# Optimization experiments

Hardware: AMD Instinct MI355X
Metric: run time of the kernel (lower is better)

Reference implementation:

```python
import jax, jax.numpy as jnp
import numpy as np

N_SUPPORT = 131072
NUM_CLASSES = 1024
D = 512
NUM_LEVELS = 3
LN_EPS = 1e-5


def setup_inputs() -> dict:
    key = jax.random.key(0)
    ks = jax.random.split(key, 10)
    s = 1.0 / np.sqrt(D)
    return {
        "support_features": jax.random.normal(ks[0], (N_SUPPORT, D), dtype=jnp.float32),
        "support_labels": jax.random.randint(ks[1], (N_SUPPORT,), 0, NUM_CLASSES, dtype=jnp.int32),
        "W1": jax.random.normal(ks[2], (NUM_LEVELS, D, D), dtype=jnp.float32) * s,
        "b1": jnp.zeros((NUM_LEVELS, D), dtype=jnp.float32),
        "ln_gamma": jnp.ones((NUM_LEVELS, D), dtype=jnp.float32),
        "ln_beta": jnp.zeros((NUM_LEVELS, D), dtype=jnp.float32),
        "W2": jax.random.normal(ks[3], (NUM_LEVELS, D, D), dtype=jnp.float32) * s,
        "b2": jnp.zeros((NUM_LEVELS, D), dtype=jnp.float32),
        "level_temperatures": jnp.ones((NUM_LEVELS,), dtype=jnp.float32),
    }


def _prototype_level(x, labels, w1, bb1, gamma, beta, w2, bb2, counts):
    # MLP: Linear -> LayerNorm -> ReLU -> (Dropout=identity, eval) -> Linear
    h = x @ w1 + bb1                                   # [N, D]
    mu = jnp.mean(h, axis=-1, keepdims=True)
    var = jnp.mean(jnp.square(h - mu), axis=-1, keepdims=True)
    h = (h - mu) * jax.lax.rsqrt(var + LN_EPS) * gamma + beta
    h = jax.nn.relu(h)
    h = h @ w2 + bb2                                   # [N, D]
    # per-class mean prototype (segment mean)
    sums = jax.ops.segment_sum(h, labels, num_segments=NUM_CLASSES)  # [C, D]
    return sums / counts


def reference(support_features, support_labels, W1, b1, ln_gamma, ln_beta, W2, b2, level_temperatures):
    labels = support_labels.astype(jnp.int32)
    counts = jax.ops.segment_sum(
        jnp.ones((support_features.shape[0],), dtype=support_features.dtype),
        labels, num_segments=NUM_CLASSES)
    counts = jnp.maximum(counts, 1.0)[:, None]         # [C, 1]

    level_protos = jax.vmap(
        lambda w1, bb1, g, bt, w2, bb2: _prototype_level(
            support_features, labels, w1, bb1, g, bt, w2, bb2, counts)
    )(W1, b1, ln_gamma, ln_beta, W2, b2)               # [L, C, D]

    level_weights = jax.nn.softmax(level_temperatures)  # [L]
    final_prototypes = jnp.einsum('l,lcd->cd', level_weights, level_protos)
    return final_prototypes
```

## Files before the change

kernel.cpp:

```cpp
#include <hip/hip_runtime.h>
#include <hip/hip_bf16.h>
#include <cstdint>

#define N_SUPPORT 131072
#define NUM_CLASSES 1024
#define DIM 512
#define LN_EPS 1e-5f

typedef __attribute__((ext_vector_type(8))) short bf16x8;
typedef __attribute__((ext_vector_type(4))) float f32x4;

__device__ __forceinline__ unsigned short f2bf(float f) {
  union { float f; uint32_t u; } c; c.f = f;
  uint32_t u = c.u;
  u += 0x7fffu + ((u >> 16) & 1u);
  return (unsigned short)(u >> 16);
}

__device__ __forceinline__ void gload16(const void* g, void* l) {
  __builtin_amdgcn_global_load_lds((const __attribute__((address_space(1))) void*)g,
                                   (__attribute__((address_space(3))) void*)l,
                                   16, 0, 0);
}

__global__ void k_hist(const int* __restrict__ labels, int* __restrict__ counts) {
  const int i = blockIdx.x * 256 + threadIdx.x;
  atomicAdd(&counts[labels[i]], 1);
}

__global__ void k_scan(const int* __restrict__ counts, int* __restrict__ offs,
                       float* __restrict__ invc) {
  __shared__ int tmp[1024];
  const int t = threadIdx.x;
  const int myc = counts[t];
  tmp[t] = myc;
  __syncthreads();
  for (int o = 1; o < 1024; o <<= 1) {
    int v = (t >= o) ? tmp[t - o] : 0;
    __syncthreads();
    tmp[t] += v;
    __syncthreads();
  }
  offs[t] = tmp[t] - myc;
  invc[t] = 1.0f / (float)max(myc, 1);
}

__global__ void k_scatter(const int* __restrict__ labels, const int* __restrict__ offs,
                          int* __restrict__ cursor, int* __restrict__ sorted) {
  const int i = blockIdx.x * 256 + threadIdx.x;
  const int c = labels[i];
  const int p = atomicAdd(&cursor[c], 1);
  sorted[offs[c] + p] = i;
}

__global__ void k_cast_sorted(const float* __restrict__ x, const int* __restrict__ sorted,
                              const int* __restrict__ labels,
                              unsigned short* __restrict__ xb, int* __restrict__ scls) {
  const int p = blockIdx.x * 4 + (threadIdx.x >> 6);
  const int src = sorted[p];
  const int k = (threadIdx.x & 63) * 8;
  const float* xr = x + (size_t)src * DIM + k;
  float4 a = *(const float4*)(xr);
  float4 b = *(const float4*)(xr + 4);
  uint4 o;
  o.x = (uint32_t)f2bf(a.x) | ((uint32_t)f2bf(a.y) << 16);
  o.y = (uint32_t)f2bf(a.z) | ((uint32_t)f2bf(a.w) << 16);
  o.z = (uint32_t)f2bf(b.x) | ((uint32_t)f2bf(b.y) << 16);
  o.w = (uint32_t)f2bf(b.z) | ((uint32_t)f2bf(b.w) << 16);
  *(uint4*)(xb + (size_t)p * DIM + k) = o;
  if ((threadIdx.x & 63) == 0) scls[p] = labels[src];
}

__global__ void k_prep_w1t(const float* __restrict__ w1, unsigned short* __restrict__ w1t) {
  const int idx = blockIdx.x * 256 + threadIdx.x;
  const int l = idx >> 18;
  const int rem = idx & 262143;
  const int k = rem >> 9;
  const int n = rem & 511;
  w1t[((size_t)l * 512 + n) * 512 + k] = f2bf(w1[idx]);
}

__global__ __launch_bounds__(256, 2) void k_gemm1lnred(
    const unsigned short* __restrict__ Xb, const unsigned short* __restrict__ W1T,
    const float* __restrict__ b1, const float* __restrict__ gamma, const float* __restrict__ beta,
    const int* __restrict__ scls_g, float* __restrict__ M, int l)
{
  __shared__ unsigned short sX[64 * 32];
  __shared__ unsigned short sW[512 * 32];
  __shared__ float wsum[4][64];
  __shared__ float wsq[4][64];
  __shared__ float smean[64];
  __shared__ float srstd[64];
  __shared__ int scls[64];
  __shared__ int run_start[65];
  __shared__ int run_cls[64];
  __shared__ int nruns_s;

  const int t = threadIdx.x;
  const int wv = t >> 6;
  const int lane = t & 63;
  const int lr = lane & 15;
  const int lq = lane >> 4;
  const int row0 = blockIdx.x * 64;

  const unsigned short* Wl = W1T + (size_t)l * 512 * 512;

  f32x4 acc[4][8];
  #pragma unroll
  for (int i = 0; i < 4; ++i)
    #pragma unroll
    for (int j = 0; j < 8; ++j) acc[i][j] = (f32x4){0.f, 0.f, 0.f, 0.f};

  const int xrow = t >> 2;
  const int ko8 = (t & 3) * 8;
  const unsigned short* xg = Xb + (size_t)(row0 + xrow) * 512 + ko8;
  unsigned short* sXw = sX + wv * 512;

  if (t < 64) scls[t] = scls_g[row0 + t];

  for (int ks = 0; ks < 16; ++ks) {
    const int kk = ks * 32;
    gload16(xg + kk, sXw);
    #pragma unroll
    for (int i = 0; i < 8; ++i) {
      const int n = i * 64 + (t >> 2);
      gload16(Wl + (size_t)n * 512 + kk + ko8, sW + (i * 256 + wv * 64) * 8);
    }
    __syncthreads();

    bf16x8 a[4], b[8];
    #pragma unroll
    for (int rf = 0; rf < 4; ++rf)
      a[rf] = *(const bf16x8*)(sX + (rf * 16 + lr) * 32 + lq * 8);
    #pragma unroll
    for (int cf = 0; cf < 8; ++cf)
      b[cf] = *(const bf16x8*)(sW + (wv * 128 + cf * 16 + lr) * 32 + lq * 8);

    #pragma unroll
    for (int rf = 0; rf < 4; ++rf)
      #pragma unroll
      for (int cf = 0; cf < 8; ++cf)
        acc[rf][cf] = __builtin_amdgcn_mfma_f32_16x16x32_bf16(a[rf], b[cf], acc[rf][cf], 0, 0, 0);
    __syncthreads();
  }

  float b1v[8], gv[8], bv[8];
  #pragma unroll
  for (int cf = 0; cf < 8; ++cf) {
    const int col = wv * 128 + cf * 16 + lr;
    b1v[cf] = b1[l * 512 + col];
    gv[cf] = gamma[l * 512 + col];
    bv[cf] = beta[l * 512 + col];
  }
  #pragma unroll
  for (int rf = 0; rf < 4; ++rf)
    #pragma unroll
    for (int cf = 0; cf < 8; ++cf)
      #pragma unroll
      for (int j = 0; j < 4; ++j) acc[rf][cf][j] += b1v[cf];

  #pragma unroll
  for (int rf = 0; rf < 4; ++rf) {
    #pragma unroll
    for (int j = 0; j < 4; ++j) {
      float s = 0.f, q = 0.f;
      #pragma unroll
      for (int cf = 0; cf < 8; ++cf) { float v = acc[rf][cf][j]; s += v; q += v * v; }
      #pragma unroll
      for (int m = 8; m >= 1; m >>= 1) { s += __shfl_xor(s, m, 16); q += __shfl_xor(q, m, 16); }
      if (lr == 0) { const int row = rf * 16 + lq * 4 + j; wsum[wv][row] = s; wsq[wv][row] = q; }
    }
  }
  __syncthreads();
  if (t < 64) {
    const float s = wsum[0][t] + wsum[1][t] + wsum[2][t] + wsum[3][t];
    const float q = wsq[0][t] + wsq[1][t] + wsq[2][t] + wsq[3][t];
    const float mean = s * (1.0f / 512.0f);
    const float var = q * (1.0f / 512.0f) - mean * mean;
    smean[t] = mean;
    srstd[t] = rsqrtf(var + LN_EPS);
  }
  if (t == 0) {
    int n = 0;
    run_start[0] = 0;
    run_cls[0] = scls[0];
    for (int r = 1; r < 64; ++r) {
      if (scls[r] != scls[r - 1]) { ++n; run_start[n] = r; run_cls[n] = scls[r]; }
    }
    nruns_s = n + 1;
    run_start[n + 1] = 64;
  }
  __syncthreads();

  #pragma unroll
  for (int rf = 0; rf < 4; ++rf) {
    #pragma unroll
    for (int j = 0; j < 4; ++j) {
      const int row = rf * 16 + lq * 4 + j;
      const float mean = smean[row], rs = srstd[row];
      #pragma unroll
      for (int cf = 0; cf < 8; ++cf) {
        float v = (acc[rf][cf][j] - mean) * rs * gv[cf] + bv[cf];
        acc[rf][cf][j] = fmaxf(v, 0.f);
      }
    }
  }

  const int nruns = nruns_s;
  float* Ml = M + (size_t)l * NUM_CLASSES * DIM;
  for (int r = 0; r < nruns; ++r) {
    const int rs = run_start[r], re = run_start[r + 1];
    const int cls = run_cls[r];
    float p[8];
    #pragma unroll
    for (int cf = 0; cf < 8; ++cf) p[cf] = 0.f;
    #pragma unroll
    for (int rf = 0; rf < 4; ++rf) {
      #pragma unroll
      for (int j = 0; j < 4; ++j) {
        const int row = rf * 16 + lq * 4 + j;
        if (row >= rs && row < re) {
          #pragma unroll
          for (int cf = 0; cf < 8; ++cf) p[cf] += acc[rf][cf][j];
        }
      }
    }
    #pragma unroll
    for (int cf = 0; cf < 8; ++cf) {
      p[cf] += __shfl_xor(p[cf], 16);
      p[cf] += __shfl_xor(p[cf], 32);
    }
    if (lq == 0) {
      #pragma unroll
      for (int cf = 0; cf < 8; ++cf)
        atomicAdd(&Ml[(size_t)cls * DIM + wv * 128 + cf * 16 + lr], p[cf]);
    }
  }
}

__global__ void k_final(const float* __restrict__ M, const float* __restrict__ W2,
                        const float* __restrict__ b2, const float* __restrict__ temps,
                        const float* __restrict__ invc, float* __restrict__ out)
{
  __shared__ float sA[64][17];
  __shared__ float sB[16][65];
  const int t = threadIdx.x;
  const int tx = t & 15, ty = t >> 4;
  const int bcol = blockIdx.x * 64;
  const int brow = blockIdx.y * 64;

  const float t0 = temps[0], t1 = temps[1], t2 = temps[2];
  const float mx = fmaxf(t0, fmaxf(t1, t2));
  const float e0 = expf(t0 - mx), e1 = expf(t1 - mx), e2 = expf(t2 - mx);
  const float inv = 1.f / (e0 + e1 + e2);
  const float w[3] = {e0 * inv, e1 * inv, e2 * inv};

  float acc[4][4] = {};
  for (int l = 0; l < 3; ++l) {
    for (int k0 = 0; k0 < 512; k0 += 16) {
      __syncthreads();
      #pragma unroll
      for (int i = 0; i < 4; ++i) {
        const int e = i * 256 + t;
        const int r = e >> 4, k = e & 15;
        sA[r][k] = M[((size_t)l * 1024 + brow + r) * 512 + k0 + k] * (w[l] * invc[brow + r]);
      }
      #pragma unroll
      for (int i = 0; i < 4; ++i) {
        const int e = i * 256 + t;
        const int r = e >> 6, nn = e & 63;
        sB[r][nn] = W2[((size_t)l * 512 + k0 + r) * 512 + bcol + nn];
      }
      __syncthreads();
      #pragma unroll
      for (int kk = 0; kk < 16; ++kk) {
        float a[4], b[4];
        #pragma unroll
        for (int i = 0; i < 4; ++i) a[i] = sA[ty * 4 + i][kk];
        #pragma unroll
        for (int j = 0; j < 4; ++j) b[j] = sB[kk][tx * 4 + j];
        #pragma unroll
        for (int i = 0; i < 4; ++i)
          #pragma unroll
          for (int j = 0; j < 4; ++j) acc[i][j] += a[i] * b[j];
      }
    }
  }
  #pragma unroll
  for (int j = 0; j < 4; ++j) {
    const int col = bcol + tx * 4 + j;
    const float bias = w[0] * b2[col] + w[1] * b2[512 + col] + w[2] * b2[1024 + col];
    #pragma unroll
    for (int i = 0; i < 4; ++i)
      out[(size_t)(brow + ty * 4 + i) * 512 + col] = acc[i][j] + bias;
  }
}

extern "C" void kernel_launch(void* const* d_in, const int* in_sizes, int n_in,
                              void* d_out, int out_size, void* d_ws, size_t ws_size,
                              hipStream_t stream)
{
  const float* X = (const float*)d_in[0];
  const int* labels = (const int*)d_in[1];
  const float* W1 = (const float*)d_in[2];
  const float* b1 = (const float*)d_in[3];
  const float* gamma = (const float*)d_in[4];
  const float* beta = (const float*)d_in[5];
  const float* W2 = (const float*)d_in[6];
  const float* b2 = (const float*)d_in[7];
  const float* temps = (const float*)d_in[8];
  float* out = (float*)d_out;

  char* ws = (char*)d_ws;
  size_t off = 0;
  auto alloc = [&](size_t bytes) -> char* {
    char* p = ws + off;
    off += (bytes + 255) & ~(size_t)255;
    return p;
  };
  unsigned short* Xb = (unsigned short*)alloc((size_t)N_SUPPORT * DIM * 2);
  unsigned short* W1T = (unsigned short*)alloc((size_t)3 * 512 * 512 * 2);
  float* M = (float*)alloc((size_t)3 * 1024 * 512 * 4);
  int* counts = (int*)alloc(2048 * 4);
  int* cursor = counts + 1024;
  int* offs = (int*)alloc(1024 * 4);
  float* invc = (float*)alloc(1024 * 4);
  int* sorted = (int*)alloc((size_t)N_SUPPORT * 4);
  int* scls = (int*)alloc((size_t)N_SUPPORT * 4);

  hipMemsetAsync(counts, 0, 2048 * 4, stream);
  hipMemsetAsync(M, 0, (size_t)3 * 1024 * 512 * 4, stream);
  k_hist<<<512, 256, 0, stream>>>(labels, counts);
  k_scan<<<1, 1024, 0, stream>>>(counts, offs, invc);
  k_scatter<<<512, 256, 0, stream>>>(labels, offs, cursor, sorted);
  k_cast_sorted<<<32768, 256, 0, stream>>>(X, sorted, labels, Xb, scls);
  k_prep_w1t<<<3072, 256, 0, stream>>>(W1, W1T);
  for (int l = 0; l < 3; ++l) {
    k_gemm1lnred<<<2048, 256, 0, stream>>>(Xb, W1T, b1, gamma, beta, scls, M, l);
  }
  k_final<<<dim3(8, 16), 256, 0, stream>>>(M, W2, b2, temps, invc, out);
}
```

Baseline: 954.3 us.

## Pre-tile X and W1 into MFMA-friendly layout, merge level launches, split final GEMM

Writes X and W1 into a k-slice-major tiled bf16 layout, so each global-to-LDS load in the GEMM is fully contiguous and the LDS fragment reads avoid the strided row layout. The three per-level GEMM launches become one 2D grid with the level on x, so the three blocks sharing an X tile run close together and can reuse it from L2. The final GEMM is split across levels in blockIdx.z and accumulates into a zeroed output with atomics, which raises parallelism from 128 blocks to 384. The costs are an extra memset, float atomic nondeterminism, and less coalesced stores in the cast and transpose kernels.

```diff
diff --git a/kernel.cpp b/kernel.cpp
--- a/kernel.cpp
+++ b/kernel.cpp
@@ -55,38 +55,57 @@
 
 __global__ void k_cast_sorted(const float* __restrict__ x, const int* __restrict__ sorted,
                               const int* __restrict__ labels,
-                              unsigned short* __restrict__ xb, int* __restrict__ scls) {
-  const int p = blockIdx.x * 4 + (threadIdx.x >> 6);
+                              unsigned short* __restrict__ xbt, int* __restrict__ scls) {
+  const int tile = blockIdx.x;
+  const int t = threadIdx.x;
+  const int rr = t & 63, ksl = t >> 6;
+  const int p = tile * 64 + rr;
   const int src = sorted[p];
-  const int k = (threadIdx.x & 63) * 8;
-  const float* xr = x + (size_t)src * DIM + k;
-  float4 a = *(const float4*)(xr);
-  float4 b = *(const float4*)(xr + 4);
+  if (t < 64) scls[p] = labels[src];
+  const float* xr = x + (size_t)src * DIM;
+  #pragma unroll
+  for (int kb = 0; kb < 4; ++kb) {
+    const int ks = kb * 4 + ksl;
+    float4 f[8];
+    #pragma unroll
+    for (int i = 0; i < 8; ++i) f[i] = *(const float4*)(xr + ks * 32 + i * 4);
+    #pragma unroll
+    for (int g = 0; g < 4; ++g) {
+      uint4 o;
+      o.x = (uint32_t)f2bf(f[g * 2].x) | ((uint32_t)f2bf(f[g * 2].y) << 16);
+      o.y = (uint32_t)f2bf(f[g * 2].z) | ((uint32_t)f2bf(f[g * 2].w) << 16);
+      o.z = (uint32_t)f2bf(f[g * 2 + 1].x) | ((uint32_t)f2bf(f[g * 2 + 1].y) << 16);
+      o.w = (uint32_t)f2bf(f[g * 2 + 1].z) | ((uint32_t)f2bf(f[g * 2 + 1].w) << 16);
+      *(uint4*)(xbt + ((size_t)(tile * 64 + ks * 4 + g)) * 512 + rr * 8) = o;
+    }
+  }
+}
+
+__global__ void k_prep_w1t(const float* __restrict__ w1, unsigned short* __restrict__ w1t) {
+  const int i = blockIdx.x * 256 + threadIdx.x;
+  const int l = i >> 15;
+  const int ks = (i >> 11) & 15;
+  const int g = (i >> 9) & 3;
+  const int n = i & 511;
+  const float* src = w1 + ((size_t)l * 512 + ks * 32 + g * 8) * 512 + n;
+  unsigned short v[8];
+  #pragma unroll
+  for (int e = 0; e < 8; ++e) v[e] = f2bf(src[(size_t)e * 512]);
   uint4 o;
-  o.x = (uint32_t)f2bf(a.x) | ((uint32_t)f2bf(a.y) << 16);
-  o.y = (uint32_t)f2bf(a.z) | ((uint32_t)f2bf(a.w) << 16);
-  o.z = (uint32_t)f2bf(b.x) | ((uint32_t)f2bf(b.y) << 16);
-  o.w = (uint32_t)f2bf(b.z) | ((uint32_t)f2bf(b.w) << 16);
-  *(uint4*)(xb + (size_t)p * DIM + k) = o;
-  if ((threadIdx.x & 63) == 0) scls[p] = labels[src];
-}
-
-__global__ void k_prep_w1t(const float* __restrict__ w1, unsigned short* __restrict__ w1t) {
-  const int idx = blockIdx.x * 256 + threadIdx.x;
-  const int l = idx >> 18;
-  const int rem = idx & 262143;
-  const int k = rem >> 9;
-  const int n = rem & 511;
-  w1t[((size_t)l * 512 + n) * 512 + k] = f2bf(w1[idx]);
+  o.x = (uint32_t)v[0] | ((uint32_t)v[1] << 16);
+  o.y = (uint32_t)v[2] | ((uint32_t)v[3] << 16);
+  o.z = (uint32_t)v[4] | ((uint32_t)v[5] << 16);
+  o.w = (uint32_t)v[6] | ((uint32_t)v[7] << 16);
+  *(uint4*)(w1t + (size_t)i * 8) = o;
 }
 
 __global__ __launch_bounds__(256, 2) void k_gemm1lnred(
-    const unsigned short* __restrict__ Xb, const unsigned short* __restrict__ W1T,
+    const unsigned short* __restrict__ XbT, const unsigned short* __restrict__ W1T,
     const float* __restrict__ b1, const float* __restrict__ gamma, const float* __restrict__ beta,
-    const int* __restrict__ scls_g, float* __restrict__ M, int l)
+    const int* __restrict__ scls_g, float* __restrict__ M)
 {
-  __shared__ unsigned short sX[64 * 32];
-  __shared__ unsigned short sW[512 * 32];
+  __shared__ unsigned short sX[4 * 64 * 8];
+  __shared__ unsigned short sW[4 * 512 * 8];
   __shared__ float wsum[4][64];
   __shared__ float wsq[4][64];
   __shared__ float smean[64];
@@ -101,9 +120,12 @@
   const int lane = t & 63;
   const int lr = lane & 15;
   const int lq = lane >> 4;
-  const int row0 = blockIdx.x * 64;
-
-  const unsigned short* Wl = W1T + (size_t)l * 512 * 512;
+  const int l = blockIdx.x;
+  const int tile = blockIdx.y;
+  const int row0 = tile * 64;
+
+  const unsigned short* xsrc = XbT + (size_t)tile * 32768;
+  const unsigned short* wsrc = W1T + (size_t)l * 262144;
 
   f32x4 acc[4][8];
   #pragma unroll
@@ -111,30 +133,23 @@
     #pragma unroll
     for (int j = 0; j < 8; ++j) acc[i][j] = (f32x4){0.f, 0.f, 0.f, 0.f};
 
-  const int xrow = t >> 2;
-  const int ko8 = (t & 3) * 8;
-  const unsigned short* xg = Xb + (size_t)(row0 + xrow) * 512 + ko8;
+  if (t < 64) scls[t] = scls_g[row0 + t];
+
   unsigned short* sXw = sX + wv * 512;
-
-  if (t < 64) scls[t] = scls_g[row0 + t];
-
   for (int ks = 0; ks < 16; ++ks) {
-    const int kk = ks * 32;
-    gload16(xg + kk, sXw);
-    #pragma unroll
-    for (int i = 0; i < 8; ++i) {
-      const int n = i * 64 + (t >> 2);
-      gload16(Wl + (size_t)n * 512 + kk + ko8, sW + (i * 256 + wv * 64) * 8);
-    }
+    gload16(xsrc + (size_t)ks * 2048 + t * 8, sXw);
+    #pragma unroll
+    for (int i = 0; i < 8; ++i)
+      gload16(wsrc + (size_t)ks * 16384 + (i * 256 + t) * 8, sW + (i * 256 + wv * 64) * 8);
     __syncthreads();
 
     bf16x8 a[4], b[8];
     #pragma unroll
     for (int rf = 0; rf < 4; ++rf)
-      a[rf] = *(const bf16x8*)(sX + (rf * 16 + lr) * 32 + lq * 8);
+      a[rf] = *(const bf16x8*)(sX + (lq * 64 + rf * 16 + lr) * 8);
     #pragma unroll
     for (int cf = 0; cf < 8; ++cf)
-      b[cf] = *(const bf16x8*)(sW + (wv * 128 + cf * 16 + lr) * 32 + lq * 8);
+      b[cf] = *(const bf16x8*)(sW + (lq * 512 + wv * 128 + cf * 16 + lr) * 8);
 
     #pragma unroll
     for (int rf = 0; rf < 4; ++rf)
@@ -248,51 +263,52 @@
   const int tx = t & 15, ty = t >> 4;
   const int bcol = blockIdx.x * 64;
   const int brow = blockIdx.y * 64;
+  const int l = blockIdx.z;
 
   const float t0 = temps[0], t1 = temps[1], t2 = temps[2];
   const float mx = fmaxf(t0, fmaxf(t1, t2));
   const float e0 = expf(t0 - mx), e1 = expf(t1 - mx), e2 = expf(t2 - mx);
   const float inv = 1.f / (e0 + e1 + e2);
   const float w[3] = {e0 * inv, e1 * inv, e2 * inv};
+  const float wl = w[l];
 
   float acc[4][4] = {};
-  for (int l = 0; l < 3; ++l) {
-    for (int k0 = 0; k0 < 512; k0 += 16) {
-      __syncthreads();
-      #pragma unroll
-      for (int i = 0; i < 4; ++i) {
-        const int e = i * 256 + t;
-        const int r = e >> 4, k = e & 15;
-        sA[r][k] = M[((size_t)l * 1024 + brow + r) * 512 + k0 + k] * (w[l] * invc[brow + r]);
-      }
-      #pragma unroll
-      for (int i = 0; i < 4; ++i) {
-        const int e = i * 256 + t;
-        const int r = e >> 6, nn = e & 63;
-        sB[r][nn] = W2[((size_t)l * 512 + k0 + r) * 512 + bcol + nn];
-      }
-      __syncthreads();
-      #pragma unroll
-      for (int kk = 0; kk < 16; ++kk) {
-        float a[4], b[4];
+  for (int k0 = 0; k0 < 512; k0 += 16) {
+    __syncthreads();
+    #pragma unroll
+    for (int i = 0; i < 4; ++i) {
+      const int e = i * 256 + t;
+      const int r = e >> 4, k = e & 15;
+      sA[r][k] = M[((size_t)l * 1024 + brow + r) * 512 + k0 + k] * (wl * invc[brow + r]);
+    }
+    #pragma unroll
+    for (int i = 0; i < 4; ++i) {
+      const int e = i * 256 + t;
+      const int r = e >> 6, nn = e & 63;
+      sB[r][nn] = W2[((size_t)l * 512 + k0 + r) * 512 + bcol + nn];
+    }
+    __syncthreads();
+    #pragma unroll
+    for (int kk = 0; kk < 16; ++kk) {
+      float a[4], b[4];
+      #pragma unroll
+      for (int i = 0; i < 4; ++i) a[i] = sA[ty * 4 + i][kk];
+      #pragma unroll
+      for (int j = 0; j < 4; ++j) b[j] = sB[kk][tx * 4 + j];
+      #pragma unroll
+      for (int i = 0; i < 4; ++i)
         #pragma unroll
-        for (int i = 0; i < 4; ++i) a[i] = sA[ty * 4 + i][kk];
-        #pragma unroll
-        for (int j = 0; j < 4; ++j) b[j] = sB[kk][tx * 4 + j];
-        #pragma unroll
-        for (int i = 0; i < 4; ++i)
-          #pragma unroll
-          for (int j = 0; j < 4; ++j) acc[i][j] += a[i] * b[j];
-      }
+        for (int j = 0; j < 4; ++j) acc[i][j] += a[i] * b[j];
     }
   }
   #pragma unroll
   for (int j = 0; j < 4; ++j) {
     const int col = bcol + tx * 4 + j;
-    const float bias = w[0] * b2[col] + w[1] * b2[512 + col] + w[2] * b2[1024 + col];
+    const float bias = (l == 0)
+        ? (w[0] * b2[col] + w[1] * b2[512 + col] + w[2] * b2[1024 + col]) : 0.f;
     #pragma unroll
     for (int i = 0; i < 4; ++i)
-      out[(size_t)(brow + ty * 4 + i) * 512 + col] = acc[i][j] + bias;
+      atomicAdd(&out[(size_t)(brow + ty * 4 + i) * 512 + col], acc[i][j] + bias);
   }
 }
 
@@ -318,7 +334,7 @@
     off += (bytes + 255) & ~(size_t)255;
     return p;
   };
-  unsigned short* Xb = (unsigned short*)alloc((size_t)N_SUPPORT * DIM * 2);
+  unsigned short* XbT = (unsigned short*)alloc((size_t)N_SUPPORT * DIM * 2);
   unsigned short* W1T = (unsigned short*)alloc((size_t)3 * 512 * 512 * 2);
   float* M = (float*)alloc((size_t)3 * 1024 * 512 * 4);
   int* counts = (int*)alloc(2048 * 4);
@@ -330,13 +346,12 @@
 
   hipMemsetAsync(counts, 0, 2048 * 4, stream);
   hipMemsetAsync(M, 0, (size_t)3 * 1024 * 512 * 4, stream);
+  hipMemsetAsync(out, 0, (size_t)NUM_CLASSES * DIM * 4, stream);
   k_hist<<<512, 256, 0, stream>>>(labels, counts);
   k_scan<<<1, 1024, 0, stream>>>(counts, offs, invc);
   k_scatter<<<512, 256, 0, stream>>>(labels, offs, cursor, sorted);
-  k_cast_sorted<<<32768, 256, 0, stream>>>(X, sorted, labels, Xb, scls);
-  k_prep_w1t<<<3072, 256, 0, stream>>>(W1, W1T);
-  for (int l = 0; l < 3; ++l) {
-    k_gemm1lnred<<<2048, 256, 0, stream>>>(Xb, W1T, b1, gamma, beta, scls, M, l);
-  }
-  k_final<<<dim3(8, 16), 256, 0, stream>>>(M, W2, b2, temps, invc, out);
-}
+  k_cast_sorted<<<2048, 256, 0, stream>>>(X, sorted, labels, XbT, scls);
+  k_prep_w1t<<<384, 256, 0, stream>>>(W1, W1T);
+  k_gemm1lnred<<<dim3(3, 2048), 256, 0, stream>>>(XbT, W1T, b1, gamma, beta, scls, M);
+  k_final<<<dim3(8, 16, 3), 256, 0, stream>>>(M, W2, b2, temps, invc, out);
+}
```

Measured after the change: 856.0 us. -10.3%, faster.
